# Optimization experiments

Measured on AMD Instinct MI355X. Metric: run time of the kernel, lower is better.

Reference implementation:

```python
import jax, jax.numpy as jnp
import numpy as np

T_ITERS, N_SLOTS, INPUT_DIM, DIM = 6, 256, 1024, 1024
MLP_DIM = DIM // 2
B, C, H, W = 8, 1024, 64, 64
LN_EPS = 1e-5


def _ln(x, g, b):
    m = jnp.mean(x, axis=-1, keepdims=True)
    v = jnp.mean(jnp.square(x - m), axis=-1, keepdims=True)
    return (x - m) * jax.lax.rsqrt(v + LN_EPS) * g + b


def setup_inputs() -> dict:
    key = jax.random.key(0)
    ks = jax.random.split(key, 8)
    x = jax.random.normal(ks[0], (B, C, H, W), dtype=jnp.float32)
    templates_init = jax.random.normal(ks[1], (1, N_SLOTS, DIM), dtype=jnp.float32)
    # torch Linear weight is [out,in]; store as [in,out] for x @ W
    s_in = 1.0 / np.sqrt(INPUT_DIM)
    s_d = 1.0 / np.sqrt(DIM)
    Wq = jax.random.uniform(ks[2], (DIM, DIM), jnp.float32, -s_d, s_d)
    Wk = jax.random.uniform(ks[3], (INPUT_DIM, DIM), jnp.float32, -s_in, s_in)
    Wv = jax.random.uniform(ks[4], (INPUT_DIM, DIM), jnp.float32, -s_in, s_in)
    W1 = jax.random.uniform(ks[5], (DIM, MLP_DIM), jnp.float32, -s_d, s_d)
    b1 = jnp.zeros((MLP_DIM,), jnp.float32)
    s_m = 1.0 / np.sqrt(MLP_DIM)
    W2 = jax.random.uniform(ks[6], (MLP_DIM, DIM), jnp.float32, -s_m, s_m)
    b2 = jnp.zeros((DIM,), jnp.float32)
    return {
        "x": x, "templates_init": templates_init,
        "Wq": Wq, "Wk": Wk, "Wv": Wv,
        "ln_in_g": jnp.ones((INPUT_DIM,), jnp.float32), "ln_in_b": jnp.zeros((INPUT_DIM,), jnp.float32),
        "ln_t_g": jnp.ones((DIM,), jnp.float32), "ln_t_b": jnp.zeros((DIM,), jnp.float32),
        "ln_m_g": jnp.ones((DIM,), jnp.float32), "ln_m_b": jnp.zeros((DIM,), jnp.float32),
        "W1": W1, "b1": b1, "W2": W2, "b2": b2,
    }


def reference(x, templates_init, Wq, Wk, Wv, ln_in_g, ln_in_b, ln_t_g, ln_t_b,
              ln_m_g, ln_m_b, W1, b1, W2, b2):
    Bv, Cv, Hv, Wd = x.shape
    scale = DIM ** (-0.5)
    xr = x.reshape(Bv, Cv, Hv * Wd).transpose(0, 2, 1)  # [B, L, C]
    xn = _ln(xr, ln_in_g, ln_in_b)
    k = xn @ Wk  # [B, L, D]
    v = xn @ Wv  # [B, L, D]
    templates = jnp.broadcast_to(templates_init, (Bv, N_SLOTS, DIM))
    attn = None
    for _ in range(T_ITERS):
        t_prev = templates
        t = _ln(t_prev, ln_t_g, ln_t_b)
        q = (t @ Wq) * scale  # [B, N, D]
        logits = jnp.einsum('bnd,bld->bln', q, k)
        attn = jax.nn.softmax(logits, axis=-1) + 1e-8  # softmax over N
        attn = attn / jnp.sum(attn, axis=-2, keepdims=True)  # renorm over L
        templates = t_prev + jnp.einsum('bld,bln->bnd', v, attn)
        m = _ln(templates, ln_m_g, ln_m_b)
        templates = templates + jax.nn.relu(m @ W1 + b1) @ W2 + b2
    out_templates = templates.transpose(0, 2, 1)[:, :, :, None]  # [B, D, N, 1]
    out_attn = attn.transpose(0, 2, 1).reshape(Bv, N_SLOTS, Hv, Wd)
    return (out_templates, out_attn)
```

## Files before the change

kernel.cpp:

```cpp
#include <hip/hip_runtime.h>

#define EPS_ 1e-5f
#define SCALE_ 0.03125f

typedef __attribute__((ext_vector_type(8))) short short8;
typedef __attribute__((ext_vector_type(4))) float f32x4;
typedef unsigned short u16;

__device__ __forceinline__ float bf2f(u16 s) {
  return __uint_as_float(((unsigned int)s) << 16);
}
__device__ __forceinline__ u16 f2bf(float f) {
  unsigned int u = __float_as_uint(f);
  unsigned int r = 0x7FFFu + ((u >> 16) & 1u);
  return (u16)((u + r) >> 16);
}

__device__ __forceinline__ void gload16(const void* g, void* l) {
  __builtin_amdgcn_global_load_lds(
      (const __attribute__((address_space(1))) unsigned int*)g,
      (__attribute__((address_space(3))) unsigned int*)l, 16, 0, 0);
}

__global__ __launch_bounds__(256) void ln_part(const float* __restrict__ x,
                                               float* __restrict__ ps,
                                               float* __restrict__ ps2) {
  int tl = threadIdx.x & 63;
  int cg = threadIdx.x >> 6;
  int lblk = blockIdx.x >> 3;
  int cchunk = blockIdx.x & 7;
  int row = lblk * 64 + tl;
  int bb = row >> 12, l = row & 4095;
  const float* xp = x + (long)bb * 4194304L + l;
  int c0 = cchunk * 128 + cg;
  float s = 0.f, s2 = 0.f;
#pragma unroll
  for (int i = 0; i < 32; ++i) {
    float v = xp[(long)(c0 + i * 4) * 4096];
    s += v; s2 += v * v;
  }
  __shared__ float sh[2][4][64];
  sh[0][cg][tl] = s; sh[1][cg][tl] = s2;
  __syncthreads();
  if (threadIdx.x < 64) {
    float ts = sh[0][0][tl] + sh[0][1][tl] + sh[0][2][tl] + sh[0][3][tl];
    float t2 = sh[1][0][tl] + sh[1][1][tl] + sh[1][2][tl] + sh[1][3][tl];
    ps[cchunk * 32768 + row] = ts;
    ps2[cchunk * 32768 + row] = t2;
  }
}

__global__ __launch_bounds__(256) void ln_red(const float* __restrict__ ps,
                                              const float* __restrict__ ps2,
                                              float* __restrict__ meanp,
                                              float* __restrict__ rstdp) {
  int row = blockIdx.x * 256 + threadIdx.x;
  float s = 0.f, s2 = 0.f;
#pragma unroll
  for (int k = 0; k < 8; ++k) {
    s += ps[k * 32768 + row];
    s2 += ps2[k * 32768 + row];
  }
  float mu = s * (1.0f / 1024.0f);
  float var = s2 * (1.0f / 1024.0f) - mu * mu;
  meanp[row] = mu;
  rstdp[row] = rsqrtf(var + EPS_);
}

__global__ __launch_bounds__(256) void xn_make(const float* __restrict__ x,
                                               u16* __restrict__ xn,
                                               const float* __restrict__ meanp,
                                               const float* __restrict__ rstdp,
                                               const float* __restrict__ g,
                                               const float* __restrict__ beta) {
  __shared__ float tile[32][33];
  int b = blockIdx.z;
  int ct = blockIdx.y * 32;
  int lt = blockIdx.x * 32;
  int tx = threadIdx.x & 31, ty = threadIdx.x >> 5;
  const float* xp = x + (long)b * 4194304;
  int l = lt + tx;
  float mu = meanp[(b << 12) + l];
  float rs = rstdp[(b << 12) + l];
#pragma unroll
  for (int k = 0; k < 32; k += 8) {
    int c = ct + ty + k;
    float v = xp[(long)c * 4096 + l];
    tile[ty + k][tx] = (v - mu) * rs * g[c] + beta[c];
  }
  __syncthreads();
  u16* xq = xn + (long)b * 4194304;
#pragma unroll
  for (int k = 0; k < 32; k += 8) {
    int ll = lt + ty + k;
    xq[(long)ll * 1024 + ct + tx] = f2bf(tile[tx][ty + k]);
  }
}

__global__ __launch_bounds__(256) void transpose_f32(const float* __restrict__ src,
                                                     float* __restrict__ dst,
                                                     int R, int Cc, long sSrc, long sDst) {
  __shared__ float tile[32][33];
  int z = blockIdx.z;
  int rt = blockIdx.y * 32, ct = blockIdx.x * 32;
  int tx = threadIdx.x & 31, ty = threadIdx.x >> 5;
  const float* s = src + (long)z * sSrc;
  float* d = dst + (long)z * sDst;
#pragma unroll
  for (int k = 0; k < 32; k += 8) tile[ty + k][tx] = s[(long)(rt + ty + k) * Cc + ct + tx];
  __syncthreads();
#pragma unroll
  for (int k = 0; k < 32; k += 8) d[(long)(ct + ty + k) * R + rt + tx] = tile[tx][ty + k];
}

__global__ __launch_bounds__(256) void tcast(const float* __restrict__ src,
                                             u16* __restrict__ dst, int R, int C) {
  __shared__ float tile[32][33];
  int rt = blockIdx.y * 32, ct = blockIdx.x * 32;
  int tx = threadIdx.x & 31, ty = threadIdx.x >> 5;
#pragma unroll
  for (int k = 0; k < 32; k += 8) tile[ty + k][tx] = src[(long)(rt + ty + k) * C + ct + tx];
  __syncthreads();
#pragma unroll
  for (int k = 0; k < 32; k += 8) dst[(long)(ct + ty + k) * R + rt + tx] = f2bf(tile[tx][ty + k]);
}

__global__ __launch_bounds__(256) void castbf(const float* __restrict__ in,
                                              u16* __restrict__ out) {
  long i = (long)blockIdx.x * 256 + threadIdx.x;
  out[i] = f2bf(in[i]);
}

enum { E_BF16 = 0, E_SCALEBF = 1, E_F32 = 2, E_UPD = 3, E_RELU = 4, E_ADDB = 5 };

template <int EPI, int KSPLIT = 1>
__global__ __launch_bounds__(256) void mgemm(
    const u16* __restrict__ A, const u16* __restrict__ Bt, void* __restrict__ Cv,
    int K, int lda, int ldb, int ldc, long sA, long sB, long sC,
    const float* __restrict__ bias, const float* __restrict__ colsum) {
  __shared__ u16 Als[128 * 64];
  __shared__ u16 Bls[128 * 64];
  const int tid = threadIdx.x;
  const int zb = (KSPLIT == 1) ? blockIdx.z : blockIdx.z / KSPLIT;
  const int ks = (KSPLIT == 1) ? 0 : blockIdx.z % KSPLIT;
  const int bm = blockIdx.y * 128;
  const int bn = blockIdx.x * 128;
  A += (long)zb * sA;
  Bt += (long)zb * sB;
  const int kpart = K / KSPLIT;
  const int kbase = ks * kpart;
  const int lane = tid & 63;
  const int w = tid >> 6;
  const int wm = (w & 1) * 64, wn = (w >> 1) * 64;
  const int fr = lane & 15;
  const int fq = lane >> 4;
  f32x4 acc[4][4] = {};

  const int srow = tid >> 3;
  const int sko = (tid & 7) << 3;
  const u16* Ag = A + (long)(bm + srow) * lda + kbase + sko;
  const u16* Bg = Bt + (long)(bn + srow) * ldb + kbase + sko;
  u16* Al = Als + tid * 8;
  u16* Bl = Bls + tid * 8;
  const long astep = 32L * lda;
  const long bstep = 32L * ldb;

  for (int k0 = 0; k0 < kpart; k0 += 64) {
#pragma unroll
    for (int i = 0; i < 4; ++i) {
      gload16(Ag + i * astep + k0, Al + i * 2048);
      gload16(Bg + i * bstep + k0, Bl + i * 2048);
    }
    __syncthreads();
#pragma unroll
    for (int kc = 0; kc < 2; ++kc) {
      const int koff = kc * 32 + fq * 8;
      short8 af[4], bf[4];
#pragma unroll
      for (int i = 0; i < 4; ++i)
        af[i] = *(const short8*)&Als[(wm + i * 16 + fr) * 64 + koff];
#pragma unroll
      for (int j = 0; j < 4; ++j)
        bf[j] = *(const short8*)&Bls[(wn + j * 16 + fr) * 64 + koff];
#pragma unroll
      for (int i = 0; i < 4; ++i)
#pragma unroll
        for (int j = 0; j < 4; ++j)
          acc[i][j] = __builtin_amdgcn_mfma_f32_16x16x32_bf16(af[i], bf[j], acc[i][j], 0, 0, 0);
    }
    __syncthreads();
  }

#pragma unroll
  for (int i = 0; i < 4; ++i) {
#pragma unroll
    for (int j = 0; j < 4; ++j) {
      int gc = bn + wn + j * 16 + fr;
#pragma unroll
      for (int r = 0; r < 4; ++r) {
        int gr = bm + wm + i * 16 + fq * 4 + r;
        float v = acc[i][j][r];
        if constexpr (EPI == E_BF16) {
          ((u16*)Cv + (long)zb * sC)[(long)gr * ldc + gc] = f2bf(v);
        } else if constexpr (EPI == E_SCALEBF) {
          ((u16*)Cv + (long)zb * sC)[(long)gr * ldc + gc] = f2bf(v * SCALE_);
        } else if constexpr (EPI == E_F32) {
          ((float*)Cv + (long)zb * sC)[(long)gr * ldc + gc] = v;
        } else if constexpr (EPI == E_UPD) {
          float* C = (float*)Cv + (long)zb * sC;
          float add = v * (1.0f / colsum[zb * 256 + gr]);
          if constexpr (KSPLIT > 1) atomicAdd(&C[(long)gr * ldc + gc], add);
          else C[(long)gr * ldc + gc] += add;
        } else if constexpr (EPI == E_RELU) {
          float h = v + bias[gc];
          ((u16*)Cv + (long)zb * sC)[(long)gr * ldc + gc] = f2bf(h > 0.f ? h : 0.f);
        } else {
          float* C = (float*)Cv + (long)zb * sC;
          C[(long)gr * ldc + gc] += v + bias[gc];
        }
      }
    }
  }
}

__global__ __launch_bounds__(256) void fls(const u16* __restrict__ qk,
                                           const u16* __restrict__ xn,
                                           u16* __restrict__ attnbf,
                                           float* __restrict__ colsum) {
  __shared__ u16 Als[256 * 64];
  __shared__ u16 Bls[64 * 64];
  __shared__ float sred[4][64];
  __shared__ float ssum[4][64];
  const int tid = threadIdx.x;
  const int z = blockIdx.z;
  const int l0 = blockIdx.x * 64;
  const u16* A = qk + (long)z * 262144;
  const u16* B = xn + (long)z * 4194304;
  const int lane = tid & 63;
  const int w = tid >> 6;
  const int wm = w * 64;
  const int fr = lane & 15, fq = lane >> 4;
  f32x4 acc[4][4] = {};

  const int srow = tid >> 3;
  const int sko = (tid & 7) << 3;
  const u16* Ag = A + (long)srow * 1024 + sko;
  const u16* Bg = B + (long)(l0 + srow) * 1024 + sko;
  u16* Al = Als + tid * 8;
  u16* Bl = Bls + tid * 8;

  for (int k0 = 0; k0 < 1024; k0 += 64) {
#pragma unroll
    for (int i = 0; i < 8; ++i)
      gload16(Ag + (long)i * 32768 + k0, Al + i * 2048);
#pragma unroll
    for (int i = 0; i < 2; ++i)
      gload16(Bg + (long)i * 32768 + k0, Bl + i * 2048);
    __syncthreads();
#pragma unroll
    for (int kc = 0; kc < 2; ++kc) {
      const int koff = kc * 32 + fq * 8;
      short8 af[4], bf[4];
#pragma unroll
      for (int i = 0; i < 4; ++i)
        af[i] = *(const short8*)&Als[(wm + i * 16 + fr) * 64 + koff];
#pragma unroll
      for (int j = 0; j < 4; ++j)
        bf[j] = *(const short8*)&Bls[(j * 16 + fr) * 64 + koff];
#pragma unroll
      for (int i = 0; i < 4; ++i)
#pragma unroll
        for (int j = 0; j < 4; ++j)
          acc[i][j] = __builtin_amdgcn_mfma_f32_16x16x32_bf16(af[i], bf[j], acc[i][j], 0, 0, 0);
    }
    __syncthreads();
  }

  float mj[4];
#pragma unroll
  for (int j = 0; j < 4; ++j) {
    float m = acc[0][j][0];
#pragma unroll
    for (int i = 0; i < 4; ++i)
#pragma unroll
      for (int r = 0; r < 4; ++r) m = fmaxf(m, acc[i][j][r]);
    m = fmaxf(m, __shfl_xor(m, 16));
    m = fmaxf(m, __shfl_xor(m, 32));
    mj[j] = m;
  }
  if (fq == 0) {
#pragma unroll
    for (int j = 0; j < 4; ++j) sred[w][j * 16 + fr] = mj[j];
  }
  __syncthreads();
  float M4[4];
#pragma unroll
  for (int j = 0; j < 4; ++j) {
    int c = j * 16 + fr;
    M4[j] = fmaxf(fmaxf(sred[0][c], sred[1][c]), fmaxf(sred[2][c], sred[3][c]));
  }
  float pj[4] = {0.f, 0.f, 0.f, 0.f};
#pragma unroll
  for (int i = 0; i < 4; ++i)
#pragma unroll
    for (int j = 0; j < 4; ++j)
#pragma unroll
      for (int r = 0; r < 4; ++r) {
        float e = __expf(acc[i][j][r] - M4[j]);
        acc[i][j][r] = e;
        pj[j] += e;
      }
#pragma unroll
  for (int j = 0; j < 4; ++j) {
    pj[j] += __shfl_xor(pj[j], 16);
    pj[j] += __shfl_xor(pj[j], 32);
  }
  if (fq == 0) {
#pragma unroll
    for (int j = 0; j < 4; ++j) ssum[w][j * 16 + fr] = pj[j];
  }
  __syncthreads();
  float inv[4];
#pragma unroll
  for (int j = 0; j < 4; ++j) {
    int c = j * 16 + fr;
    inv[j] = 1.0f / (ssum[0][c] + ssum[1][c] + ssum[2][c] + ssum[3][c]);
  }
  u16* outp = attnbf + (long)z * 1048576;
#pragma unroll
  for (int i = 0; i < 4; ++i) {
#pragma unroll
    for (int r = 0; r < 4; ++r) {
      int n = wm + i * 16 + fq * 4 + r;
      float cs = 0.f;
#pragma unroll
      for (int j = 0; j < 4; ++j) {
        float a = acc[i][j][r] * inv[j] + 1e-8f;
        u16 ab = f2bf(a);
        outp[(long)n * 4096 + l0 + j * 16 + fr] = ab;
        cs += bf2f(ab);
      }
      cs += __shfl_xor(cs, 1);
      cs += __shfl_xor(cs, 2);
      cs += __shfl_xor(cs, 4);
      cs += __shfl_xor(cs, 8);
      if (fr == 0) atomicAdd(&colsum[z * 256 + n], cs);
    }
  }
}

__global__ __launch_bounds__(256) void row_ln_bf(const float* __restrict__ in,
                                                 u16* __restrict__ out,
                                                 const float* __restrict__ g,
                                                 const float* __restrict__ bvec,
                                                 float* __restrict__ cz) {
  if (cz && blockIdx.x < 8) cz[blockIdx.x * 256 + threadIdx.x] = 0.f;
  long base = (long)blockIdx.x * 1024;
  int c = threadIdx.x << 2;
  float4 xv = *(const float4*)&in[base + c];
  float s = xv.x + xv.y + xv.z + xv.w;
  float s2 = xv.x * xv.x + xv.y * xv.y + xv.z * xv.z + xv.w * xv.w;
#pragma unroll
  for (int off = 32; off > 0; off >>= 1) {
    s += __shfl_down(s, off);
    s2 += __shfl_down(s2, off);
  }
  __shared__ float sh[8];
  if ((threadIdx.x & 63) == 0) {
    sh[threadIdx.x >> 6] = s;
    sh[4 + (threadIdx.x >> 6)] = s2;
  }
  __syncthreads();
  float ts = sh[0] + sh[1] + sh[2] + sh[3];
  float t2 = sh[4] + sh[5] + sh[6] + sh[7];
  float mu = ts * (1.0f / 1024.0f);
  float rs = rsqrtf(t2 * (1.0f / 1024.0f) - mu * mu + EPS_);
  ushort4 o;
  o.x = f2bf((xv.x - mu) * rs * g[c + 0] + bvec[c + 0]);
  o.y = f2bf((xv.y - mu) * rs * g[c + 1] + bvec[c + 1]);
  o.z = f2bf((xv.z - mu) * rs * g[c + 2] + bvec[c + 2]);
  o.w = f2bf((xv.w - mu) * rs * g[c + 3] + bvec[c + 3]);
  *(ushort4*)&out[base + c] = o;
}

__global__ __launch_bounds__(256) void bcast_tmpl(const float* __restrict__ tinit,
                                                  float* __restrict__ tmpl) {
  long i = (long)blockIdx.x * 256 + threadIdx.x;
  tmpl[i] = tinit[i & 262143];
}

__global__ __launch_bounds__(256) void attn_final_g(const u16* __restrict__ ab,
                                                    const float* __restrict__ cs,
                                                    float* __restrict__ out) {
  long i = (long)blockIdx.x * 256 + threadIdx.x;
  out[i] = bf2f(ab[i]) / cs[i >> 12];
}

extern "C" void kernel_launch(void* const* d_in, const int* in_sizes, int n_in,
                              void* d_out, int out_size, void* d_ws, size_t ws_size,
                              hipStream_t stream) {
  const float* x       = (const float*)d_in[0];
  const float* tinit   = (const float*)d_in[1];
  const float* Wq      = (const float*)d_in[2];
  const float* Wk      = (const float*)d_in[3];
  const float* Wv      = (const float*)d_in[4];
  const float* ln_in_g = (const float*)d_in[5];
  const float* ln_in_b = (const float*)d_in[6];
  const float* ln_t_g  = (const float*)d_in[7];
  const float* ln_t_b  = (const float*)d_in[8];
  const float* ln_m_g  = (const float*)d_in[9];
  const float* ln_m_b  = (const float*)d_in[10];
  const float* W1      = (const float*)d_in[11];
  const float* b1      = (const float*)d_in[12];
  const float* W2      = (const float*)d_in[13];
  const float* b2      = (const float*)d_in[14];
  (void)in_sizes; (void)n_in; (void)out_size; (void)ws_size;

  char* ws = (char*)d_ws;
  size_t off = 0;
  auto alloc = [&](size_t bytes) {
    void* p = ws + off;
    off += (bytes + 255) & ~(size_t)255;
    return p;
  };
  float* meanp   = (float*)alloc(32768ULL * 4);
  float* rstdp   = (float*)alloc(32768ULL * 4);
  float* ps      = (float*)alloc(262144ULL * 4);
  float* ps2     = (float*)alloc(262144ULL * 4);
  u16* xn        = (u16*)alloc(33554432ULL * 2);
  u16* vT        = (u16*)alloc(33554432ULL * 2);
  u16* attnbf    = (u16*)alloc(8388608ULL * 2);
  u16* tln       = (u16*)alloc(2097152ULL * 2);
  u16* qk        = (u16*)alloc(2097152ULL * 2);
  u16* hidden    = (u16*)alloc(1048576ULL * 2);
  float* tmpl    = (float*)alloc(2097152ULL * 4);
  u16* WqkT      = (u16*)alloc(1048576ULL * 2);
  u16* WvT       = (u16*)alloc(1048576ULL * 2);
  u16* W1T       = (u16*)alloc(524288ULL * 2);
  u16* W2T       = (u16*)alloc(524288ULL * 2);
  float* colsum  = (float*)alloc(2048ULL * 4);

  u16* Wkbf = attnbf;
  u16* Wqbf = attnbf + 1048576;

  float* outT        = (float*)d_out;
  float* attnOutBase = (float*)d_out + 2097152;

  dim3 blk(256);

  ln_part<<<dim3(4096), blk, 0, stream>>>(x, ps, ps2);
  ln_red<<<dim3(128), blk, 0, stream>>>(ps, ps2, meanp, rstdp);

  castbf<<<dim3(4096), blk, 0, stream>>>(Wk, Wkbf);
  castbf<<<dim3(4096), blk, 0, stream>>>(Wq, Wqbf);
  mgemm<E_SCALEBF><<<dim3(8, 8, 1), blk, 0, stream>>>(
      Wkbf, Wqbf, WqkT, 1024, 1024, 1024, 1024, 0, 0, 0, nullptr, nullptr);
  tcast<<<dim3(32, 32), blk, 0, stream>>>(Wv, WvT, 1024, 1024);
  tcast<<<dim3(16, 32), blk, 0, stream>>>(W1, W1T, 1024, 512);
  tcast<<<dim3(32, 16), blk, 0, stream>>>(W2, W2T, 512, 1024);

  xn_make<<<dim3(128, 32, 8), blk, 0, stream>>>(x, xn, meanp, rstdp, ln_in_g, ln_in_b);
  mgemm<E_BF16><<<dim3(32, 8, 8), blk, 0, stream>>>(
      WvT, xn, vT, 1024, 1024, 1024, 4096, 0, 4194304L, 4194304L, nullptr, nullptr);
  bcast_tmpl<<<dim3(8192), blk, 0, stream>>>(tinit, tmpl);

  for (int it = 0; it < 6; ++it) {
    row_ln_bf<<<dim3(2048), blk, 0, stream>>>(tmpl, tln, ln_t_g, ln_t_b, colsum);
    mgemm<E_BF16><<<dim3(8, 16, 1), blk, 0, stream>>>(
        tln, WqkT, qk, 1024, 1024, 1024, 1024, 0, 0, 0, nullptr, nullptr);
    fls<<<dim3(64, 1, 8), blk, 0, stream>>>(qk, xn, attnbf, colsum);
    mgemm<E_UPD, 2><<<dim3(8, 2, 16), blk, 0, stream>>>(
        attnbf, vT, tmpl, 4096, 4096, 4096, 1024, 1048576L, 4194304L, 262144L,
        nullptr, colsum);
    row_ln_bf<<<dim3(2048), blk, 0, stream>>>(tmpl, tln, ln_m_g, ln_m_b, nullptr);
    mgemm<E_RELU><<<dim3(4, 16, 1), blk, 0, stream>>>(
        tln, W1T, hidden, 1024, 1024, 1024, 512, 0, 0, 0, b1, nullptr);
    mgemm<E_ADDB><<<dim3(8, 16, 1), blk, 0, stream>>>(
        hidden, W2T, tmpl, 512, 512, 512, 1024, 0, 0, 0, b2, nullptr);
  }

  attn_final_g<<<dim3(32768), blk, 0, stream>>>(attnbf, colsum, attnOutBase);
  transpose_f32<<<dim3(32, 8, 8), blk, 0, stream>>>(
      tmpl, outT, 256, 1024, 262144L, 262144L);
}
```

Measured before the change: 1.439 ms.

## Double-buffer LDS tiles in bf16 MFMA GEMM to overlap loads with compute

The GEMM kernel now uses two LDS buffers for A and B tiles and issues global-to-LDS loads for the next K step before computing on the current one. This hides global load latency behind MFMA work and halves the barriers per K step. It doubles LDS usage to 64 KB per block, which may lower occupancy. It also assumes an even number of 64-wide K steps, at least two.

```diff
diff --git a/kernel.cpp b/kernel.cpp
--- a/kernel.cpp
+++ b/kernel.cpp
@@ -138,8 +138,8 @@
     const u16* __restrict__ A, const u16* __restrict__ Bt, void* __restrict__ Cv,
     int K, int lda, int ldb, int ldc, long sA, long sB, long sC,
     const float* __restrict__ bias, const float* __restrict__ colsum) {
-  __shared__ u16 Als[128 * 64];
-  __shared__ u16 Bls[128 * 64];
+  __shared__ u16 Als[2][128 * 64];
+  __shared__ u16 Bls[2][128 * 64];
   const int tid = threadIdx.x;
   const int zb = (KSPLIT == 1) ? blockIdx.z : blockIdx.z / KSPLIT;
   const int ks = (KSPLIT == 1) ? 0 : blockIdx.z % KSPLIT;
@@ -160,36 +160,50 @@
   const int sko = (tid & 7) << 3;
   const u16* Ag = A + (long)(bm + srow) * lda + kbase + sko;
   const u16* Bg = Bt + (long)(bn + srow) * ldb + kbase + sko;
-  u16* Al = Als + tid * 8;
-  u16* Bl = Bls + tid * 8;
   const long astep = 32L * lda;
   const long bstep = 32L * ldb;
 
-  for (int k0 = 0; k0 < kpart; k0 += 64) {
-#pragma unroll
-    for (int i = 0; i < 4; ++i) {
-      gload16(Ag + i * astep + k0, Al + i * 2048);
-      gload16(Bg + i * bstep + k0, Bl + i * 2048);
-    }
+#define STAGE_(bufI, kOff)                                                   \
+  {                                                                          \
+    _Pragma("unroll") for (int i_ = 0; i_ < 4; ++i_) {                       \
+      gload16(Ag + i_ * astep + (kOff), &Als[bufI][tid * 8 + i_ * 2048]);    \
+      gload16(Bg + i_ * bstep + (kOff), &Bls[bufI][tid * 8 + i_ * 2048]);    \
+    }                                                                        \
+  }
+
+#define COMPUTE_(bufI)                                                       \
+  {                                                                          \
+    _Pragma("unroll") for (int kc = 0; kc < 2; ++kc) {                       \
+      const int koff = kc * 32 + fq * 8;                                     \
+      short8 af[4], bv[4];                                                   \
+      _Pragma("unroll") for (int i = 0; i < 4; ++i)                          \
+          af[i] = *(const short8*)&Als[bufI][(wm + i * 16 + fr) * 64 + koff];\
+      _Pragma("unroll") for (int j = 0; j < 4; ++j)                          \
+          bv[j] = *(const short8*)&Bls[bufI][(wn + j * 16 + fr) * 64 + koff];\
+      _Pragma("unroll") for (int i = 0; i < 4; ++i)                          \
+          _Pragma("unroll") for (int j = 0; j < 4; ++j)                      \
+              acc[i][j] = __builtin_amdgcn_mfma_f32_16x16x32_bf16(           \
+                  af[i], bv[j], acc[i][j], 0, 0, 0);                         \
+    }                                                                        \
+  }
+
+  const int nsteps = kpart >> 6;
+  STAGE_(0, 0);
+  __syncthreads();
+  for (int s = 0; s < nsteps - 2; s += 2) {
+    STAGE_(1, (s + 1) * 64);
+    COMPUTE_(0);
     __syncthreads();
-#pragma unroll
-    for (int kc = 0; kc < 2; ++kc) {
-      const int koff = kc * 32 + fq * 8;
-      short8 af[4], bf[4];
-#pragma unroll
-      for (int i = 0; i < 4; ++i)
-        af[i] = *(const short8*)&Als[(wm + i * 16 + fr) * 64 + koff];
-#pragma unroll
-      for (int j = 0; j < 4; ++j)
-        bf[j] = *(const short8*)&Bls[(wn + j * 16 + fr) * 64 + koff];
-#pragma unroll
-      for (int i = 0; i < 4; ++i)
-#pragma unroll
-        for (int j = 0; j < 4; ++j)
-          acc[i][j] = __builtin_amdgcn_mfma_f32_16x16x32_bf16(af[i], bf[j], acc[i][j], 0, 0, 0);
-    }
+    STAGE_(0, (s + 2) * 64);
+    COMPUTE_(1);
     __syncthreads();
   }
+  STAGE_(1, (nsteps - 1) * 64);
+  COMPUTE_(0);
+  __syncthreads();
+  COMPUTE_(1);
+#undef STAGE_
+#undef COMPUTE_
 
 #pragma unroll
   for (int i = 0; i < 4; ++i) {
```

Measured after the change: 1.381 ms. 4.0% less time.
